# Optimization experiments

Measured on AMD Instinct MI355X. Metric: run time of the kernel, lower is better.

The kernel has to match this reference:

```python
import jax, jax.numpy as jnp
import numpy as np

N_FREQ = 256
N_CH = 256
VOCAB = 8192
B, T = 4, 2048


def gauss_proj(x, w, n_freq):
    # FFT over vocab dim, take first n_freq harmonics (skip DC), split real/imag
    X = jnp.fft.rfft(x, axis=-1)[..., 1:n_freq + 1]          # [B,T,n_freq] complex
    X_ri = jnp.concatenate([X.real, X.imag], axis=-1)         # [B,T,2*n_freq]
    return X_ri @ w.T                                         # [B,T,n_channels]


def gauss_synth(h, w, n_freq, V):
    Y_ri = h @ w                                              # [B,T,2*n_freq]
    Y = Y_ri[..., :n_freq] + 1j * Y_ri[..., n_freq:]          # [B,T,n_freq] complex
    full = jnp.zeros(h.shape[:-1] + (V // 2 + 1,), dtype=Y.dtype)
    full = full.at[..., 1:n_freq + 1].set(Y)                  # band-limited spectrum
    return jnp.fft.irfft(full, n=V, axis=-1)                  # [B,T,V]


def setup_inputs() -> dict:
    key = jax.random.key(0)
    ks = jax.random.split(key, 5)
    x = jax.random.normal(ks[0], (B, T, VOCAB), dtype=jnp.float32)
    q_w = jax.random.normal(ks[1], (N_CH, 2 * N_FREQ), dtype=jnp.float32) * 0.02
    k_w = jax.random.normal(ks[2], (N_CH, 2 * N_FREQ), dtype=jnp.float32) * 0.02
    v_w = jax.random.normal(ks[3], (N_CH, 2 * N_FREQ), dtype=jnp.float32) * 0.02
    o_w = jax.random.normal(ks[4], (N_CH, 2 * N_FREQ), dtype=jnp.float32) * 0.02
    decay_logit = jnp.float32(3.0)
    out_scale = jnp.float32(0.1)
    return {"x": x, "q_w": q_w, "k_w": k_w, "v_w": v_w, "o_w": o_w,
            "decay_logit": decay_logit, "out_scale": out_scale}


def reference(x, q_w, k_w, v_w, o_w, decay_logit, out_scale):
    q = gauss_proj(x, q_w, N_FREQ)                            # [B,T,C]
    k = gauss_proj(x, k_w, N_FREQ)
    v = gauss_proj(x, v_w, N_FREQ)
    scores = jnp.einsum('btc,bsc->bts', q, k)                 # [B,T,T]
    decay = jax.nn.sigmoid(decay_logit)
    t = x.shape[1]
    pos = jnp.arange(t)
    # faithful to torch: diff[t,s] = pos[s] - pos[t]
    diff = pos[None, :] - pos[:, None]
    weights = (decay ** jnp.clip(diff.astype(jnp.float32) - 1.0, 0.0)) * (diff > 0)
    scores = scores * weights[None, :, :]
    retrieved = jnp.einsum('bts,bsc->btc', scores, v)         # [B,T,C]
    return gauss_synth(retrieved, o_w, N_FREQ, VOCAB) * out_scale
```

## Files before the change

kernel.cpp:

```cpp
#include <hip/hip_runtime.h>
#include <hip/hip_bf16.h>
#include <cstdint>


typedef unsigned short u16;
typedef short short8 __attribute__((ext_vector_type(8)));
typedef float f32x4 __attribute__((ext_vector_type(4)));
typedef float f4 __attribute__((ext_vector_type(4)));

__device__ __forceinline__ u16 f2bf(float f) {
  union { float f; unsigned u; } v; v.f = f;
  unsigned u = v.u;
  u += 0x7fffu + ((u >> 16) & 1u);
  return (u16)(u >> 16);
}

__device__ __forceinline__ uint2 pack_bf4(f4 v) {
  union { u16 h[4]; uint2 q; } pk;
  pk.h[0] = f2bf(v[0]); pk.h[1] = f2bf(v[1]);
  pk.h[2] = f2bf(v[2]); pk.h[3] = f2bf(v[3]);
  return pk.q;
}

__device__ __forceinline__ void gload_lds16(const void* g, void* l) {
  __builtin_amdgcn_global_load_lds(
      (const __attribute__((address_space(1))) void*)g,
      (__attribute__((address_space(3))) void*)l, 16, 0, 0);
}

__global__ __launch_bounds__(256, 2)
void gemm_g1(const float* __restrict__ A, const u16* __restrict__ B,
             float* __restrict__ P)
{
  constexpr int NN = 512, KK = 8192, KC = 4096;
  constexpr int NT = KC / 32;

  __shared__ u16 As[2][128 * 32] __attribute__((aligned(16)));
  __shared__ u16 Bs[2][128 * 32] __attribute__((aligned(16)));

  const int tid  = threadIdx.x;
  const int wave = tid >> 6, lane = tid & 63;
  const int quad = lane >> 4, l15 = lane & 15;
  const int wm = wave >> 1, wn = wave & 1;

  const int lid = blockIdx.x;
  const int nat = (lid & 7) * 64 + (lid >> 3);
  const int y = nat >> 3, rem = nat & 7;
  const int x = rem & 3, z = rem >> 2;
  const int m0 = y * 128, n0 = x * 128, k00 = z * KC;

  const int loff0 = wave * 2048 + lane * 16;
  const int loff1 = loff0 + 1024;
  const int row0s = loff0 >> 6, kof0 = (loff0 & 63) >> 1;
  const int row1s = loff1 >> 6, kof1 = (loff1 & 63) >> 1;
  const u16* Bp0 = B + (size_t)(n0 + row0s) * KK + k00 + kof0;
  const u16* Bp1 = B + (size_t)(n0 + row1s) * KK + k00 + kof1;

  const int arow8 = tid >> 3;
  const int acol  = (tid & 7) * 4;
  const float* Ap = A + (size_t)(m0 + arow8) * KK + k00 + acol;

  f4 pv[4];

  #pragma unroll
  for (int g = 0; g < 4; ++g)
    pv[g] = *(const f4*)(Ap + (size_t)g * 32 * KK);
  gload_lds16(Bp0, (char*)Bs[0] + loff0);
  gload_lds16(Bp1, (char*)Bs[0] + loff1);
  #pragma unroll
  for (int g = 0; g < 4; ++g)
    *(uint2*)&As[0][(g * 32 + arow8) * 32 + acol] = pack_bf4(pv[g]);
  __syncthreads();

  f32x4 acc[4][4] = {};

#define G1_COMPUTE(CUR)                                                          \
  {                                                                              \
    short8 a[4], b[4];                                                           \
    _Pragma("unroll")                                                            \
    for (int i = 0; i < 4; ++i)                                                  \
      a[i] = *(const short8*)&As[CUR][(wm * 64 + i * 16 + l15) * 32 + quad * 8]; \
    _Pragma("unroll")                                                            \
    for (int j = 0; j < 4; ++j)                                                  \
      b[j] = *(const short8*)&Bs[CUR][(wn * 64 + j * 16 + l15) * 32 + quad * 8]; \
    _Pragma("unroll")                                                            \
    for (int i = 0; i < 4; ++i)                                                  \
      _Pragma("unroll")                                                          \
      for (int j = 0; j < 4; ++j)                                                \
        acc[i][j] = __builtin_amdgcn_mfma_f32_16x16x32_bf16(a[i], b[j], acc[i][j], 0, 0, 0); \
  }

  for (int t = 0; t < NT - 1; ++t) {
    const int cur = t & 1, nxt = cur ^ 1;
    #pragma unroll
    for (int g = 0; g < 4; ++g)
      pv[g] = *(const f4*)(Ap + (size_t)g * 32 * KK + (t + 1) * 32);
    gload_lds16(Bp0 + (t + 1) * 32, (char*)Bs[nxt] + loff0);
    gload_lds16(Bp1 + (t + 1) * 32, (char*)Bs[nxt] + loff1);

    G1_COMPUTE(cur);

    #pragma unroll
    for (int g = 0; g < 4; ++g)
      *(uint2*)&As[nxt][(g * 32 + arow8) * 32 + acol] = pack_bf4(pv[g]);
    __syncthreads();
  }

  G1_COMPUTE((NT - 1) & 1);
#undef G1_COMPUTE

  float* Pz = P + (size_t)z * (8192L * 512);
  #pragma unroll
  for (int i = 0; i < 4; ++i) {
    #pragma unroll
    for (int j = 0; j < 4; ++j) {
      const int rb = m0 + wm * 64 + i * 16 + quad * 4;
      const int cc = n0 + wn * 64 + j * 16 + l15;
      #pragma unroll
      for (int r = 0; r < 4; ++r)
        Pz[(size_t)(rb + r) * NN + cc] = acc[i][j][r];
    }
  }
}

__global__ void reduce_cast(const float* __restrict__ P, u16* __restrict__ Xri) {
  const int i = blockIdx.x * 256 + threadIdx.x;
  const f4 a = ((const f4*)P)[i];
  const f4 b = ((const f4*)(P + 8192L * 512))[i];
  union { u16 h[4]; uint2 q; } pk;
  #pragma unroll
  for (int r = 0; r < 4; ++r) pk.h[r] = f2bf(a[r] + b[r]);
  ((uint2*)Xri)[i] = pk.q;
}

__global__ __launch_bounds__(256, 2)
void gemm_qkvw(const u16* __restrict__ Xri, const u16* __restrict__ Fm,
               const u16* __restrict__ qwb, const u16* __restrict__ kwb,
               const u16* __restrict__ vwb, const u16* __restrict__ owb,
               u16* __restrict__ Qb, u16* __restrict__ Kb,
               u16* __restrict__ Vt, u16* __restrict__ Wot)
{
  constexpr int N = 256, K = 512;
  __shared__ u16 As[128 * 32] __attribute__((aligned(16)));
  __shared__ u16 Bs[128 * 32] __attribute__((aligned(16)));

  const int tid  = threadIdx.x;
  const int wave = tid >> 6, lane = tid & 63;
  const int quad = lane >> 4, l15 = lane & 15;
  const int wm = wave >> 1, wn = wave & 1;
  const int m0 = blockIdx.y * 128, n0 = blockIdx.x * 128;
  const int z  = blockIdx.z;

  const u16* Ab = (z == 3) ? Fm : Xri;
  const u16* Bb = (z == 0) ? qwb : (z == 1) ? kwb : (z == 2) ? vwb : owb;
  const float alpha = (z == 3) ? (2.f / 8192.f) : 1.f;

  f32x4 acc[4][4] = {};

  const int loff0 = wave * 2048 + lane * 16;
  const int loff1 = loff0 + 1024;
  const int row0s = loff0 >> 6, kof0 = (loff0 & 63) >> 1;
  const int row1s = loff1 >> 6, kof1 = (loff1 & 63) >> 1;

  for (int k0 = 0; k0 < K; k0 += 32) {
    __syncthreads();
    gload_lds16(Ab + (size_t)(m0 + row0s) * K + k0 + kof0, (char*)As + loff0);
    gload_lds16(Ab + (size_t)(m0 + row1s) * K + k0 + kof1, (char*)As + loff1);
    gload_lds16(Bb + (size_t)(n0 + row0s) * K + k0 + kof0, (char*)Bs + loff0);
    gload_lds16(Bb + (size_t)(n0 + row1s) * K + k0 + kof1, (char*)Bs + loff1);
    __syncthreads();

    short8 a[4], b[4];
    #pragma unroll
    for (int i = 0; i < 4; ++i)
      a[i] = *(const short8*)&As[(wm * 64 + i * 16 + l15) * 32 + quad * 8];
    #pragma unroll
    for (int j = 0; j < 4; ++j)
      b[j] = *(const short8*)&Bs[(wn * 64 + j * 16 + l15) * 32 + quad * 8];
    #pragma unroll
    for (int i = 0; i < 4; ++i)
      #pragma unroll
      for (int j = 0; j < 4; ++j)
        acc[i][j] = __builtin_amdgcn_mfma_f32_16x16x32_bf16(a[i], b[j], acc[i][j], 0, 0, 0);
  }

  #pragma unroll
  for (int i = 0; i < 4; ++i) {
    #pragma unroll
    for (int j = 0; j < 4; ++j) {
      f32x4 v = acc[i][j];
      const int rb = m0 + wm * 64 + i * 16 + quad * 4;
      const int cc = n0 + wn * 64 + j * 16 + l15;
      if (z == 2) {
        const int bb = rb >> 11, ml = rb & 2047;
        union { u16 h[4]; uint2 q; } pk;
        #pragma unroll
        for (int r = 0; r < 4; ++r) pk.h[r] = f2bf(v[r]);
        *(uint2*)&Vt[((size_t)(bb << 8) + cc) * 2048 + ml] = pk.q;
      } else {
        u16* C = (z == 0) ? Qb : (z == 1) ? Kb : Wot;
        #pragma unroll
        for (int r = 0; r < 4; ++r)
          C[(size_t)(rb + r) * N + cc] = f2bf(v[r] * alpha);
      }
    }
  }
}

template<int EPI, bool AF32>
__global__ __launch_bounds__(256, 2)
void gemm_bt(const void* __restrict__ Av, const u16* __restrict__ B,
             void* __restrict__ Cv, int M, int N, int K,
             long sA, long sB, long sC,
             const float* __restrict__ scal, float alpha)
{
  __shared__ u16 As[128 * 32] __attribute__((aligned(16)));
  __shared__ u16 Bs[128 * 32] __attribute__((aligned(16)));

  const int tid  = threadIdx.x;
  const int wave = tid >> 6, lane = tid & 63;
  const int quad = lane >> 4, l15 = lane & 15;
  const int wm = wave >> 1, wn = wave & 1;
  const int m0 = blockIdx.y * 128, n0 = blockIdx.x * 128;
  const int z  = blockIdx.z;

  const u16*   Ab = (const u16*)Av + (size_t)z * sA;
  const float* Af = (const float*)Av + (size_t)z * sA;
  const u16*   Bb = B + (size_t)z * sB;

  f32x4 acc[4][4] = {};

  const int loff0 = wave * 2048 + lane * 16;
  const int loff1 = loff0 + 1024;
  const int row0s = loff0 >> 6, kof0 = (loff0 & 63) >> 1;
  const int row1s = loff1 >> 6, kof1 = (loff1 & 63) >> 1;

  for (int k0 = 0; k0 < K; k0 += 32) {
    __syncthreads();
    if (AF32) {
      const int row = tid >> 1, half = tid & 1;
      const float* ar = Af + (size_t)(m0 + row) * K + k0 + half * 16;
      f4 p0 = *(const f4*)(ar);
      f4 p1 = *(const f4*)(ar + 4);
      f4 p2 = *(const f4*)(ar + 8);
      f4 p3 = *(const f4*)(ar + 12);
      union { u16 h[16]; uint4 q[2]; } pk;
      #pragma unroll
      for (int e = 0; e < 4; ++e) {
        pk.h[e]      = f2bf(p0[e]);
        pk.h[4 + e]  = f2bf(p1[e]);
        pk.h[8 + e]  = f2bf(p2[e]);
        pk.h[12 + e] = f2bf(p3[e]);
      }
      uint4* dst = (uint4*)&As[row * 32 + half * 16];
      dst[0] = pk.q[0]; dst[1] = pk.q[1];
    } else {
      gload_lds16(Ab + (size_t)(m0 + row0s) * K + k0 + kof0, (char*)As + loff0);
      gload_lds16(Ab + (size_t)(m0 + row1s) * K + k0 + kof1, (char*)As + loff1);
    }
    gload_lds16(Bb + (size_t)(n0 + row0s) * K + k0 + kof0, (char*)Bs + loff0);
    gload_lds16(Bb + (size_t)(n0 + row1s) * K + k0 + kof1, (char*)Bs + loff1);
    __syncthreads();

    short8 a[4], b[4];
    #pragma unroll
    for (int i = 0; i < 4; ++i)
      a[i] = *(const short8*)&As[(wm * 64 + i * 16 + l15) * 32 + quad * 8];
    #pragma unroll
    for (int j = 0; j < 4; ++j)
      b[j] = *(const short8*)&Bs[(wn * 64 + j * 16 + l15) * 32 + quad * 8];
    #pragma unroll
    for (int i = 0; i < 4; ++i)
      #pragma unroll
      for (int j = 0; j < 4; ++j)
        acc[i][j] = __builtin_amdgcn_mfma_f32_16x16x32_bf16(a[i], b[j], acc[i][j], 0, 0, 0);
  }

  float dec_l2 = 0.f, oscale = 1.f;
  if (EPI == 3) {
    float logit = *scal;
    float dec = 1.f / (1.f + expf(-logit));
    dec_l2 = log2f(dec);
  }
  if (EPI == 4) oscale = *scal;

  #pragma unroll
  for (int i = 0; i < 4; ++i) {
    #pragma unroll
    for (int j = 0; j < 4; ++j) {
      f32x4 v = acc[i][j];
      const int rb = m0 + wm * 64 + i * 16 + quad * 4;
      const int cc = n0 + wn * 64 + j * 16 + l15;
      if (EPI == 0) {
        u16* C = (u16*)Cv + (size_t)z * sC;
        #pragma unroll
        for (int r = 0; r < 4; ++r)
          C[(size_t)(rb + r) * N + cc] = f2bf(v[r] * alpha);
      } else if (EPI == 2) {
        u16* C = (u16*)Cv;
        const int bb = rb >> 11, ml = rb & 2047;
        union { u16 h[4]; uint2 q; } pk;
        #pragma unroll
        for (int r = 0; r < 4; ++r) pk.h[r] = f2bf(v[r]);
        *(uint2*)&C[((size_t)(bb << 8) + cc) * 2048 + ml] = pk.q;
      } else if (EPI == 3) {
        u16* C = (u16*)Cv + (size_t)z * sC;
        #pragma unroll
        for (int r = 0; r < 4; ++r) {
          const int d = cc - (rb + r);
          float w = (d > 0) ? exp2f(dec_l2 * (float)(d - 1)) : 0.f;
          C[(size_t)(rb + r) * N + cc] = f2bf(v[r] * w);
        }
      } else if (EPI == 4) {
        float* C = (float*)Cv;
        #pragma unroll
        for (int r = 0; r < 4; ++r)
          C[(size_t)(rb + r) * N + cc] = v[r] * oscale;
      }
    }
  }
}

__global__ void genF_row(u16* Fm) {
  int idx = blockIdx.x * 256 + threadIdx.x;
  int n = idx >> 9, j = idx & 511;
  int k = (j & 255) + 1;
  int ph = (n * k) & 8191;
  float ang = (float)ph * 7.66990393942820795e-4f;
  float s, c; sincosf(ang, &s, &c);
  Fm[idx] = f2bf(j < 256 ? c : -s);
}
__global__ void genF_col(u16* Ft) {
  int idx = blockIdx.x * 256 + threadIdx.x;
  int j = idx >> 13, n = idx & 8191;
  int k = (j & 255) + 1;
  int ph = (n * k) & 8191;
  float ang = (float)ph * 7.66990393942820795e-4f;
  float s, c; sincosf(ang, &s, &c);
  Ft[idx] = f2bf(j < 256 ? c : -s);
}

__global__ void cast_w4(const float* a, const float* b, const float* c, const float* d,
                        u16* oa, u16* ob, u16* oc, u16* od) {
  int i = blockIdx.x * 256 + threadIdx.x;
  oa[i] = f2bf(a[i]); ob[i] = f2bf(b[i]); oc[i] = f2bf(c[i]); od[i] = f2bf(d[i]);
}

extern "C" void kernel_launch(void* const* d_in, const int* in_sizes, int n_in,
                              void* d_out, int out_size, void* d_ws, size_t ws_size,
                              hipStream_t stream)
{
  const float* x  = (const float*)d_in[0];
  const float* qw = (const float*)d_in[1];
  const float* kw = (const float*)d_in[2];
  const float* vw = (const float*)d_in[3];
  const float* ow = (const float*)d_in[4];
  const float* dl = (const float*)d_in[5];
  const float* os = (const float*)d_in[6];
  float* out = (float*)d_out;

  char* W = (char*)d_ws;
  const size_t MB = 1024 * 1024;
  u16* Fm  = (u16*)(W);
  u16* Ft  = (u16*)(W + 8 * MB);
  u16* Xri = (u16*)(W + 16 * MB);
  u16* Qb  = (u16*)(W + 24 * MB);
  u16* Kb  = (u16*)(W + 28 * MB);
  u16* Vt  = (u16*)(W + 32 * MB);
  u16* Wot = (u16*)(W + 36 * MB);
  u16* S   = (u16*)(W + 40 * MB);
  float* P = (float*)(W + 40 * MB);
  u16* R   = (u16*)(W + 72 * MB);
  u16* qwb = (u16*)(W + 76 * MB);
  u16* kwb = qwb + 131072;
  u16* vwb = kwb + 131072;
  u16* owb = vwb + 131072;

  genF_row<<<8192 * 512 / 256, 256, 0, stream>>>(Fm);
  genF_col<<<8192 * 512 / 256, 256, 0, stream>>>(Ft);
  cast_w4<<<131072 / 256, 256, 0, stream>>>(qw, kw, vw, ow, qwb, kwb, vwb, owb);

  gemm_g1<<<512, 256, 0, stream>>>(x, Ft, P);
  reduce_cast<<<4096, 256, 0, stream>>>(P, Xri);

  gemm_qkvw<<<dim3(2, 64, 4), 256, 0, stream>>>(Xri, Fm, qwb, kwb, vwb, owb,
                                                Qb, Kb, Vt, Wot);

  gemm_bt<3, false><<<dim3(16, 16, 4), 256, 0, stream>>>(Qb, Kb, S, 2048, 2048, 256,
                                                         2048L * 256, 2048L * 256, 2048L * 2048, dl, 1.f);
  gemm_bt<0, false><<<dim3(2, 16, 4), 256, 0, stream>>>(S, Vt, R, 2048, 256, 2048,
                                                        2048L * 2048, 256L * 2048, 2048L * 256, nullptr, 1.f);
  gemm_bt<4, false><<<dim3(64, 64, 1), 256, 0, stream>>>(R, Wot, out, 8192, 8192, 256, 0, 0, 0, os, 1.f);
}
```

Baseline: 716.1 us.

## Deepen gemm_g1 prefetch pipeline to two stages with triple-buffered B tiles

The first projection GEMM now prefetches A and B two k-steps ahead instead of one. B tiles move to a three-slot LDS ring, A register staging is split into two alternating register sets, and the barrier uses a partial vmcnt wait so the newest loads stay in flight. The aim is to hide global memory latency in this memory-bound fp32-to-bf16 GEMM, at the cost of extra LDS and registers and a redundant clamped reload at the tail.

Measured after the change: 680.5 us. 1.05x faster.

```diff
diff --git a/kernel.cpp b/kernel.cpp
--- a/kernel.cpp
+++ b/kernel.cpp
@@ -36,7 +36,7 @@
   constexpr int NT = KC / 32;
 
   __shared__ u16 As[2][128 * 32] __attribute__((aligned(16)));
-  __shared__ u16 Bs[2][128 * 32] __attribute__((aligned(16)));
+  __shared__ u16 Bs[3][128 * 32] __attribute__((aligned(16)));
 
   const int tid  = threadIdx.x;
   const int wave = tid >> 6, lane = tid & 63;
@@ -60,21 +60,20 @@
   const int acol  = (tid & 7) * 4;
   const float* Ap = A + (size_t)(m0 + arow8) * KK + k00 + acol;
 
-  f4 pv[4];
-
-  #pragma unroll
-  for (int g = 0; g < 4; ++g)
-    pv[g] = *(const f4*)(Ap + (size_t)g * 32 * KK);
-  gload_lds16(Bp0, (char*)Bs[0] + loff0);
-  gload_lds16(Bp1, (char*)Bs[0] + loff1);
-  #pragma unroll
-  for (int g = 0; g < 4; ++g)
-    *(uint2*)&As[0][(g * 32 + arow8) * 32 + acol] = pack_bf4(pv[g]);
-  __syncthreads();
-
-  f32x4 acc[4][4] = {};
-
-#define G1_COMPUTE(CUR)                                                          \
+  f4 rv0[4], rv1[4];
+
+#define ISSUE_A(RV, T)                                               \
+  _Pragma("unroll")                                                  \
+  for (int g = 0; g < 4; ++g)                                        \
+    RV[g] = *(const f4*)(Ap + (size_t)g * 32 * KK + (size_t)(T) * 32);
+#define ISSUE_B(T, SLOT)                                             \
+  gload_lds16(Bp0 + (size_t)(T) * 32, (char*)Bs[SLOT] + loff0);      \
+  gload_lds16(Bp1 + (size_t)(T) * 32, (char*)Bs[SLOT] + loff1);
+#define CONVERT_A(RV, SLOT)                                          \
+  _Pragma("unroll")                                                  \
+  for (int g = 0; g < 4; ++g)                                        \
+    *(uint2*)&As[SLOT][(g * 32 + arow8) * 32 + acol] = pack_bf4(RV[g]);
+#define G1_COMPUTE(CUR, BSLOT)                                                   \
   {                                                                              \
     short8 a[4], b[4];                                                           \
     _Pragma("unroll")                                                            \
@@ -82,32 +81,48 @@
       a[i] = *(const short8*)&As[CUR][(wm * 64 + i * 16 + l15) * 32 + quad * 8]; \
     _Pragma("unroll")                                                            \
     for (int j = 0; j < 4; ++j)                                                  \
-      b[j] = *(const short8*)&Bs[CUR][(wn * 64 + j * 16 + l15) * 32 + quad * 8]; \
+      b[j] = *(const short8*)&Bs[BSLOT][(wn * 64 + j * 16 + l15) * 32 + quad * 8]; \
     _Pragma("unroll")                                                            \
     for (int i = 0; i < 4; ++i)                                                  \
       _Pragma("unroll")                                                          \
       for (int j = 0; j < 4; ++j)                                                \
         acc[i][j] = __builtin_amdgcn_mfma_f32_16x16x32_bf16(a[i], b[j], acc[i][j], 0, 0, 0); \
   }
-
-  for (int t = 0; t < NT - 1; ++t) {
-    const int cur = t & 1, nxt = cur ^ 1;
-    #pragma unroll
-    for (int g = 0; g < 4; ++g)
-      pv[g] = *(const f4*)(Ap + (size_t)g * 32 * KK + (t + 1) * 32);
-    gload_lds16(Bp0 + (t + 1) * 32, (char*)Bs[nxt] + loff0);
-    gload_lds16(Bp1 + (t + 1) * 32, (char*)Bs[nxt] + loff1);
-
-    G1_COMPUTE(cur);
-
-    #pragma unroll
-    for (int g = 0; g < 4; ++g)
-      *(uint2*)&As[nxt][(g * 32 + arow8) * 32 + acol] = pack_bf4(pv[g]);
-    __syncthreads();
-  }
-
-  G1_COMPUTE((NT - 1) & 1);
+#define FENCE_BAR()                                                  \
+  asm volatile("s_waitcnt vmcnt(6)" ::: "memory");                   \
+  asm volatile("s_waitcnt lgkmcnt(0)" ::: "memory");                 \
+  __builtin_amdgcn_s_barrier();                                      \
+  asm volatile("" ::: "memory");
+
+  ISSUE_A(rv0, 0);
+  ISSUE_B(0, 0);
+  ISSUE_A(rv1, 1);
+  ISSUE_B(1, 1);
+  CONVERT_A(rv0, 0);
+  FENCE_BAR();
+
+  f32x4 acc[4][4] = {};
+
+#define BODY(T, RV_ISS, RV_CONV)                                     \
+  {                                                                  \
+    const int t2 = ((T) + 2 < NT) ? (T) + 2 : NT - 1;                \
+    ISSUE_A(RV_ISS, t2);                                             \
+    ISSUE_B(t2, ((T) + 2) % 3);                                      \
+    G1_COMPUTE((T) & 1, (T) % 3);                                    \
+    CONVERT_A(RV_CONV, ((T) + 1) & 1);                               \
+    FENCE_BAR();                                                     \
+  }
+
+  for (int t = 0; t < NT; t += 2) {
+    BODY(t, rv0, rv1);
+    BODY(t + 1, rv1, rv0);
+  }
+#undef BODY
+#undef FENCE_BAR
 #undef G1_COMPUTE
+#undef CONVERT_A
+#undef ISSUE_B
+#undef ISSUE_A
 
   float* Pz = P + (size_t)z * (8192L * 512);
   #pragma unroll
```
